# Performance work log

Hardware: AMD Instinct MI355X
Metric: run time of the kernel (lower is better)

The kernel has to match this reference:

```python
import jax, jax.numpy as jnp
import numpy as np

N, S, E, H = 2, 2048, 1024, 16
D = E // H  # head_dim = 64


def setup_inputs() -> dict:
    key = jax.random.key(0)
    k1, k2, k3 = jax.random.split(key, 3)
    x = jax.random.normal(k1, (N, S, E), dtype=jnp.float32)
    # Xavier-uniform-scaled weights (torch Linear layout: [out_features, in_features])
    lim_qkv = (6.0 / (E + 3 * E)) ** 0.5
    qkv_w = jax.random.uniform(k2, (3 * E, E), dtype=jnp.float32, minval=-lim_qkv, maxval=lim_qkv)
    lim_o = (6.0 / (E + E)) ** 0.5
    o_w = jax.random.uniform(k3, (E, E), dtype=jnp.float32, minval=-lim_o, maxval=lim_o)
    # causal look-ahead mask: positions where mask == 0 are excluded
    attn_mask = jnp.tril(jnp.ones((S, S), dtype=jnp.int32))
    return {"x": x, "attn_mask": attn_mask, "qkv_w": qkv_w, "o_w": o_w}


def reference(x, attn_mask, qkv_w, o_w):
    n, s, e = x.shape
    qkv = x @ qkv_w.T                              # (N, S, 3E)
    q, k, v = jnp.split(qkv, 3, axis=-1)
    # (N, S, E) -> (N, H, S, D)
    def to_heads(t):
        return t.reshape(n, s, H, D).transpose(0, 2, 1, 3)
    q, k, v = to_heads(q), to_heads(k), to_heads(v)
    scale = 1.0 / jnp.sqrt(jnp.asarray(D, dtype=x.dtype))
    logits = jnp.einsum('bhqd,bhkd->bhqk', q, k) * scale   # (N, H, S, S)
    mask = attn_mask.reshape(1, 1, s, s)                    # expand_mask: 2D -> (1,1,S,S)
    logits = jnp.where(mask == 0, -jnp.inf, logits)
    attn_weights = jax.nn.softmax(logits, axis=-1)
    values = jnp.einsum('bhqk,bhkd->bhqd', attn_weights, v)  # (N, H, S, D)
    values = values.transpose(0, 2, 1, 3).reshape(n, s, e)
    o = values @ o_w.T
    return o
```

## Files before the change

### kernel.cpp

```cpp
#include <hip/hip_runtime.h>
#include <math.h>

typedef unsigned short u16;
typedef unsigned int uint;
typedef __attribute__((ext_vector_type(8))) short bf16x8;
typedef __attribute__((ext_vector_type(8))) _Float16 half8;
typedef __attribute__((ext_vector_type(4))) float floatx4;

__device__ __forceinline__ u16 f2bf(float f) {
  union { float f; uint u; } c; c.f = f;
  return (u16)((c.u + 0x7FFFu + ((c.u >> 16) & 1u)) >> 16);
}
__device__ __forceinline__ float bf2f(u16 h) {
  union { uint u; float f; } c; c.u = ((uint)h) << 16;
  return c.f;
}
__device__ __forceinline__ u16 h2u(_Float16 h) {
  union { _Float16 h; u16 u; } c; c.h = h;
  return c.u;
}

#if __has_builtin(__builtin_amdgcn_exp2f)
#define EX2 __builtin_amdgcn_exp2f
#else
#define EX2 exp2f
#endif

__device__ __forceinline__ void gl_lds16(const u16* g, u16* l) {
  __builtin_amdgcn_global_load_lds(
      (const __attribute__((address_space(1))) uint*)g,
      (__attribute__((address_space(3))) uint*)l, 16, 0, 0);
}

__device__ __forceinline__ void store_c(u16* p, float v) { *p = f2bf(v); }
__device__ __forceinline__ void store_c(float* p, float v) { *p = v; }

#define ROR16(x, n)                                                        \
  __builtin_bit_cast(float, __builtin_amdgcn_update_dpp(                   \
      __builtin_bit_cast(int, (x)), __builtin_bit_cast(int, (x)),          \
      0x120 + (n), 0xF, 0xF, false))
__device__ __forceinline__ float rsum16(float x) {
  x += ROR16(x, 8); x += ROR16(x, 4); x += ROR16(x, 2); x += ROR16(x, 1);
  return x;
}

__global__ __launch_bounds__(256) void cvt_all(const float* __restrict__ x,
                                               const float* __restrict__ qw,
                                               const float* __restrict__ ow,
                                               u16* __restrict__ xb,
                                               u16* __restrict__ wb,
                                               u16* __restrict__ ob) {
  int bx = blockIdx.x;
  const float* src; u16* dst; int off;
  if (bx < 2048) { src = x; dst = xb; off = bx; }
  else if (bx < 3584) { src = qw; dst = wb; off = bx - 2048; }
  else { src = ow; dst = ob; off = bx - 3584; }
  int i = (off * 256 + threadIdx.x) * 8;
  float4 a = *(const float4*)(src + i);
  float4 b = *(const float4*)(src + i + 4);
  bf16x8 r;
  r[0] = (short)f2bf(a.x); r[1] = (short)f2bf(a.y);
  r[2] = (short)f2bf(a.z); r[3] = (short)f2bf(a.w);
  r[4] = (short)f2bf(b.x); r[5] = (short)f2bf(b.y);
  r[6] = (short)f2bf(b.z); r[7] = (short)f2bf(b.w);
  *(bf16x8*)(dst + i) = r;
}

__global__ __launch_bounds__(256) void vtrans(const u16* __restrict__ qkv,
                                              u16* __restrict__ vt) {
  constexpr int S = 2048, E = 1024, TE = 3072;
  __shared__ u16 tile[64 * 72];
  const int t = threadIdx.x;
  const int kv0 = blockIdx.x * 64;
  const int bh = blockIdx.y, b = bh >> 4, h = bh & 15;
  const u16* src = qkv + (size_t)b * S * TE + 2 * E + h * 64;
#pragma unroll
  for (int i = 0; i < 2; ++i) {
    int c = t + i * 256;
    int kv = c >> 3, d0 = (c & 7) * 8;
    *(bf16x8*)&tile[kv * 72 + d0] = *(const bf16x8*)&src[(size_t)(kv0 + kv) * TE + d0];
  }
  __syncthreads();
  u16* dst = vt + (size_t)bh * 64 * S + kv0;
#pragma unroll
  for (int i = 0; i < 2; ++i) {
    int c = t + i * 256;
    int d = c >> 3, k0 = (c & 7) * 8;
    bf16x8 r;
#pragma unroll
    for (int j = 0; j < 8; ++j)
      r[j] = (short)h2u((_Float16)bf2f(tile[(k0 + j) * 72 + d]));
    *(bf16x8*)&dst[(size_t)d * S + k0] = r;
  }
}

template <typename TC>
__global__ __launch_bounds__(256) void gemm_bt(const u16* __restrict__ A,
                                               const u16* __restrict__ B,
                                               TC* __restrict__ C,
                                               int K, int N) {
  __shared__ __align__(16) u16 lds_a[128 * 64];
  __shared__ __align__(16) u16 lds_b[128 * 64];
  const int t = threadIdx.x;
  const int w = t >> 6, lane = t & 63, quad = lane >> 4, lr = lane & 15;
  const int wr = w >> 1, wc = w & 1;
  const int m0 = blockIdx.y * 128, n0 = blockIdx.x * 128;

  const int srow = lane >> 3;
  const int scol = ((lane & 7) ^ srow) * 8;
  const u16* Ab = A + (size_t)(m0 + w * 32 + srow) * K + scol;
  const u16* Bb = B + (size_t)(n0 + w * 32 + srow) * K + scol;
  u16* la = lds_a + (w * 32) * 64;
  u16* lb = lds_b + (w * 32) * 64;

  floatx4 acc[4][4];
#pragma unroll
  for (int i = 0; i < 4; ++i)
#pragma unroll
    for (int j = 0; j < 4; ++j) acc[i][j] = {0.f, 0.f, 0.f, 0.f};

  for (int k0 = 0; k0 < K; k0 += 64) {
#pragma unroll
    for (int j = 0; j < 4; ++j) {
      gl_lds16(Ab + (size_t)(j * 8) * K + k0, la + j * 8 * 64);
      gl_lds16(Bb + (size_t)(j * 8) * K + k0, lb + j * 8 * 64);
    }
    __syncthreads();
#pragma unroll
    for (int kk = 0; kk < 2; ++kk) {
      bf16x8 af[4], bfr[4];
#pragma unroll
      for (int mi = 0; mi < 4; ++mi)
        af[mi] = *(const bf16x8*)&lds_a[(wr * 64 + mi * 16 + lr) * 64 +
                                        (((kk * 4 + quad) ^ (lr & 7)) * 8)];
#pragma unroll
      for (int ni = 0; ni < 4; ++ni)
        bfr[ni] = *(const bf16x8*)&lds_b[(wc * 64 + ni * 16 + lr) * 64 +
                                         (((kk * 4 + quad) ^ (lr & 7)) * 8)];
#pragma unroll
      for (int mi = 0; mi < 4; ++mi)
#pragma unroll
        for (int ni = 0; ni < 4; ++ni)
          acc[mi][ni] = __builtin_amdgcn_mfma_f32_16x16x32_bf16(
              af[mi], bfr[ni], acc[mi][ni], 0, 0, 0);
    }
    __syncthreads();
  }
#pragma unroll
  for (int mi = 0; mi < 4; ++mi)
#pragma unroll
    for (int r = 0; r < 4; ++r) {
      int m = m0 + wr * 64 + mi * 16 + quad * 4 + r;
#pragma unroll
      for (int ni = 0; ni < 4; ++ni) {
        int n = n0 + wc * 64 + ni * 16 + lr;
        store_c(&C[(size_t)m * N + n], acc[mi][ni][r]);
      }
    }
}

template <typename TC>
__global__ __launch_bounds__(256) void gemm_bt64(const u16* __restrict__ A,
                                                 const u16* __restrict__ B,
                                                 TC* __restrict__ C,
                                                 int K, int N) {
  __shared__ __align__(16) u16 lds_a[64 * 64];
  __shared__ __align__(16) u16 lds_b[128 * 64];
  const int t = threadIdx.x;
  const int w = t >> 6, lane = t & 63, quad = lane >> 4, lr = lane & 15;
  const int m0 = blockIdx.y * 64, n0 = blockIdx.x * 128;

  const int srow = lane >> 3;
  const int scol = ((lane & 7) ^ srow) * 8;
  const u16* Ab = A + (size_t)(m0 + srow) * K + scol;
  const u16* Bb = B + (size_t)(n0 + srow) * K + scol;

  floatx4 acc[4][2];
#pragma unroll
  for (int i = 0; i < 4; ++i)
#pragma unroll
    for (int j = 0; j < 2; ++j) acc[i][j] = {0.f, 0.f, 0.f, 0.f};

  for (int k0 = 0; k0 < K; k0 += 64) {
#pragma unroll
    for (int i = 0; i < 2; ++i)
      gl_lds16(Ab + (size_t)((w * 2 + i) * 8) * K + k0, &lds_a[(w * 2 + i) * 8 * 64]);
#pragma unroll
    for (int i = 0; i < 4; ++i)
      gl_lds16(Bb + (size_t)((w * 4 + i) * 8) * K + k0, &lds_b[(w * 4 + i) * 8 * 64]);
    __syncthreads();
#pragma unroll
    for (int kk = 0; kk < 2; ++kk) {
      bf16x8 af[4], bfr[2];
#pragma unroll
      for (int mi = 0; mi < 4; ++mi)
        af[mi] = *(const bf16x8*)&lds_a[(mi * 16 + lr) * 64 +
                                        (((kk * 4 + quad) ^ (lr & 7)) * 8)];
#pragma unroll
      for (int ni = 0; ni < 2; ++ni)
        bfr[ni] = *(const bf16x8*)&lds_b[(w * 32 + ni * 16 + lr) * 64 +
                                         (((kk * 4 + quad) ^ (lr & 7)) * 8)];
#pragma unroll
      for (int mi = 0; mi < 4; ++mi)
#pragma unroll
        for (int ni = 0; ni < 2; ++ni)
          acc[mi][ni] = __builtin_amdgcn_mfma_f32_16x16x32_bf16(
              af[mi], bfr[ni], acc[mi][ni], 0, 0, 0);
    }
    __syncthreads();
  }
#pragma unroll
  for (int mi = 0; mi < 4; ++mi)
#pragma unroll
    for (int r = 0; r < 4; ++r) {
      int m = m0 + mi * 16 + quad * 4 + r;
#pragma unroll
      for (int ni = 0; ni < 2; ++ni) {
        int n = n0 + w * 32 + ni * 16 + lr;
        store_c(&C[(size_t)m * N + n], acc[mi][ni][r]);
      }
    }
}

__global__ __launch_bounds__(256, 2) void attn_fwd(const u16* __restrict__ qkv,
                                                   const u16* __restrict__ vt,
                                                   u16* __restrict__ out,
                                                   float* __restrict__ opart,
                                                   float* __restrict__ lpart) {
  constexpr int S = 2048, E = 1024, TE = 3072;
  constexpr float NEG = -1e30f;
  __shared__ __align__(16) u16 lds_k[2][128 * 64];
  __shared__ __align__(16) u16 lds_vt[2][64 * 128];
  __shared__ __align__(16) u16 lds_p[4][16 * 128];
  const int t = threadIdx.x;
  const int w = t >> 6, lane = t & 63, quad = lane >> 4, lr = lane & 15;
  const int bx = (int)blockIdx.x;
  const int h = bx & 15, pr = (bx >> 4) & 7, hB = (bx >> 7) & 1, b = bx >> 8;
  const int qtH = 15 - pr;
  const int bh = b * 16 + h;
  const int pid = bh * 8 + pr;
  const size_t base = (size_t)b * S * TE;
  const u16* kbase = qkv + base + E + h * 64;
  const u16* vtb = vt + (size_t)bh * 64 * S;

  const int s8 = lane >> 3;
  const int kcol = ((lane & 7) ^ s8) * 8;
  const int vrow = lane >> 4;
  u16* const pb = &lds_p[w][0];

  const int n0 = hB ? (8 - pr) : 8;
  const int niter = hB ? 9 : 8;

  const float QS = 0.125f * 1.44269504f;
  bf16x8 qf[2][2];
  float lst[2][4];
  floatx4 oacc[2][4];

  auto load_q = [&](int qt) {
#pragma unroll
    for (int rg = 0; rg < 2; ++rg)
#pragma unroll
      for (int kk = 0; kk < 2; ++kk) {
        bf16x8 q = *(const bf16x8*)&qkv[base +
            (size_t)(qt * 128 + w * 32 + rg * 16 + lr) * TE + h * 64 + kk * 32 + quad * 8];
#pragma unroll
        for (int jj = 0; jj < 8; ++jj) q[jj] = (short)f2bf(bf2f((u16)q[jj]) * QS);
        qf[rg][kk] = q;
      }
  };
  auto reset_acc = [&]() {
#pragma unroll
    for (int rg = 0; rg < 2; ++rg) {
#pragma unroll
      for (int r = 0; r < 4; ++r) lst[rg][r] = 0.f;
#pragma unroll
      for (int di = 0; di < 4; ++di) oacc[rg][di] = {0.f, 0.f, 0.f, 0.f};
    }
  };
  auto emit_partial = [&](int slot) {
    float* op = opart + ((size_t)slot * 256 + pid) * (128 * 64);
    float* lp = lpart + ((size_t)slot * 256 + pid) * 128;
#pragma unroll
    for (int rg = 0; rg < 2; ++rg)
#pragma unroll
      for (int r = 0; r < 4; ++r) {
        int row = w * 32 + rg * 16 + quad * 4 + r;
        float lt = rsum16(lst[rg][r]);
        if (lr == 0) lp[row] = lt;
#pragma unroll
        for (int di = 0; di < 4; ++di)
          op[row * 64 + di * 16 + lr] = oacc[rg][di][r];
      }
  };
  auto kv_of = [&](int it) -> int {
    if (!hB) return it;
    return (it < n0) ? (8 + it) : (it - n0);
  };
  auto stage = [&](int kvt, int bi) {
    int nb = kvt * 128;
#pragma unroll
    for (int i = 0; i < 4; ++i) {
      int p0 = w * 8 + i * 32;
      int kv = nb + ((p0 & 15) + s8) * 8 + (p0 >> 4);
      gl_lds16(kbase + (size_t)kv * TE + kcol, &lds_k[bi][p0 * 64]);
    }
#pragma unroll
    for (int i = 0; i < 4; ++i) {
      int d0 = w * 4 + i * 16;
      int d = d0 + vrow;
      int cbg = ((lane & 15) ^ (d & 15)) * 8;
      gl_lds16(vtb + (size_t)d * S + nb + cbg, &lds_vt[bi][d0 * 128]);
    }
  };

  load_q(qtH);
  stage(kv_of(0), 0);
  reset_acc();

  for (int it = 0; it < niter; ++it) {
    const int cur = it & 1;
    const int kt = kv_of(it);
    const int qcur = (hB && it >= n0) ? pr : qtH;

    if (it + 1 < niter) {
      stage(kv_of(it + 1), cur ^ 1);
      asm volatile("s_waitcnt vmcnt(8)\n\ts_barrier" ::: "memory");
    } else {
      asm volatile("s_waitcnt vmcnt(0)\n\ts_barrier" ::: "memory");
    }
    __builtin_amdgcn_sched_barrier(0);

    floatx4 st[2][8];
#pragma unroll
    for (int rg = 0; rg < 2; ++rg)
#pragma unroll
      for (int ni = 0; ni < 8; ++ni) st[rg][ni] = {-4.f, -4.f, -4.f, -4.f};
    __builtin_amdgcn_s_setprio(1);
#pragma unroll
    for (int kk = 0; kk < 2; ++kk) {
      bf16x8 kb[8];
#pragma unroll
      for (int ni = 0; ni < 8; ++ni)
        kb[ni] = *(const bf16x8*)&lds_k[cur][(ni * 16 + lr) * 64 +
                                            (((kk * 4 + quad) ^ (lr & 7)) * 8)];
#pragma unroll
      for (int rg = 0; rg < 2; ++rg)
#pragma unroll
        for (int ni = 0; ni < 8; ++ni)
          st[rg][ni] = __builtin_amdgcn_mfma_f32_16x16x32_bf16(
              qf[rg][kk], kb[ni], st[rg][ni], 0, 0, 0);
    }
    __builtin_amdgcn_s_setprio(0);

    half8 vb[4][4];
#pragma unroll
    for (int kk = 0; kk < 4; ++kk)
#pragma unroll
      for (int di = 0; di < 4; ++di)
        vb[kk][di] = *(const half8*)&lds_vt[cur][(di * 16 + lr) * 128 +
                                                 (((kk * 4 + quad) ^ lr) << 3)];

    asm volatile("s_waitcnt lgkmcnt(0)\n\ts_barrier" ::: "memory");
    __builtin_amdgcn_sched_barrier(0);

    const bool diag = (kt == qcur);
#pragma unroll
    for (int rg = 0; rg < 2; ++rg) {
#pragma unroll
      for (int r = 0; r < 4; ++r) {
        const int rw = quad * 4 + r;
        const int rloc = w * 32 + rg * 16 + rw;
        if (diag) {
#pragma unroll
          for (int ni = 0; ni < 8; ++ni)
            if (lr * 8 + ni > rloc) st[rg][ni][r] = NEG;
        }
        float pv[8];
#pragma unroll
        for (int ni = 0; ni < 8; ++ni) pv[ni] = EX2(st[rg][ni][r]);
        lst[rg][r] += ((pv[0] + pv[1]) + (pv[2] + pv[3])) +
                      ((pv[4] + pv[5]) + (pv[6] + pv[7]));
        half8 p8;
#pragma unroll
        for (int ni = 0; ni < 8; ++ni) p8[ni] = (_Float16)pv[ni];
        *(half8*)&pb[rw * 128 + (((lr + rw) & 15) << 3)] = p8;
      }
      __builtin_amdgcn_s_setprio(1);
#pragma unroll
      for (int kk = 0; kk < 4; ++kk) {
        half8 pf = *(const half8*)&pb[lr * 128 +
                                      ((((kk * 4 + quad) + lr) & 15) << 3)];
#pragma unroll
        for (int di = 0; di < 4; ++di)
          oacc[rg][di] = __builtin_amdgcn_mfma_f32_16x16x32_f16(
              pf, vb[kk][di], oacc[rg][di], 0, 0, 0);
      }
      __builtin_amdgcn_s_setprio(0);
    }

    if (hB && it == n0 - 1) {
      emit_partial(1);
      reset_acc();
      load_q(pr);
    }
  }

  if (!hB) {
    emit_partial(0);
  } else {
#pragma unroll
    for (int rg = 0; rg < 2; ++rg)
#pragma unroll
      for (int r = 0; r < 4; ++r) {
        int sg = pr * 128 + w * 32 + rg * 16 + quad * 4 + r;
        float inv_l = 1.f / rsum16(lst[rg][r]);
#pragma unroll
        for (int di = 0; di < 4; ++di)
          out[((size_t)(b * S + sg)) * E + h * 64 + di * 16 + lr] =
              f2bf(oacc[rg][di][r] * inv_l);
      }
  }
}

__global__ __launch_bounds__(256) void attn_combine(const float* __restrict__ opart,
                                                    const float* __restrict__ lpart,
                                                    u16* __restrict__ out) {
  constexpr int S = 2048, E = 1024;
  const int p = (int)blockIdx.x;
  const int pr = p & 7, bh = p >> 3, h = bh & 15, b = bh >> 4;
  const int q0 = (15 - pr) * 128;
  const int t = threadIdx.x;
  const int row = t >> 1, c0 = (t & 1) * 32;
  const float* o0 = opart + (size_t)p * (128 * 64) + row * 64 + c0;
  const float* o1 = o0 + (size_t)256 * 128 * 64;
  float l = lpart[p * 128 + row] + lpart[256 * 128 + p * 128 + row];
  float inv = 1.f / l;
  u16* dst = out + ((size_t)(b * S + q0 + row)) * E + h * 64 + c0;
#pragma unroll
  for (int i = 0; i < 4; ++i) {
    float4 a0 = ((const float4*)o0)[2 * i], a1 = ((const float4*)o0)[2 * i + 1];
    float4 b0 = ((const float4*)o1)[2 * i], b1 = ((const float4*)o1)[2 * i + 1];
    bf16x8 r;
    r[0] = (short)f2bf((a0.x + b0.x) * inv);
    r[1] = (short)f2bf((a0.y + b0.y) * inv);
    r[2] = (short)f2bf((a0.z + b0.z) * inv);
    r[3] = (short)f2bf((a0.w + b0.w) * inv);
    r[4] = (short)f2bf((a1.x + b1.x) * inv);
    r[5] = (short)f2bf((a1.y + b1.y) * inv);
    r[6] = (short)f2bf((a1.z + b1.z) * inv);
    r[7] = (short)f2bf((a1.w + b1.w) * inv);
    ((bf16x8*)dst)[i] = r;
  }
}

extern "C" void kernel_launch(void* const* d_in, const int* in_sizes, int n_in,
                              void* d_out, int out_size, void* d_ws, size_t ws_size,
                              hipStream_t stream) {
  constexpr int NB = 2, S = 2048, E = 1024;
  constexpr int M = NB * S;
  const float* x = (const float*)d_in[0];
  const float* qkv_w = (const float*)d_in[2];
  const float* o_w = (const float*)d_in[3];
  float* out = (float*)d_out;

  u16* qkv = (u16*)d_ws;
  u16* vt = qkv + (size_t)M * 3 * E;
  u16* xb = vt + (size_t)32 * 64 * S;
  u16* attn_o = xb;
  u16* wb = xb + (size_t)M * E;
  u16* ob = wb + (size_t)3 * E * E;
  float* opart = (float*)(ob + (size_t)E * E);
  float* lpart = opart + (size_t)2 * 256 * 128 * 64;

  cvt_all<<<4096, 256, 0, stream>>>(x, qkv_w, o_w, xb, wb, ob);
  gemm_bt<u16><<<dim3(3 * E / 128, M / 128), 256, 0, stream>>>(xb, wb, qkv, E, 3 * E);
  vtrans<<<dim3(S / 64, NB * 16), 256, 0, stream>>>(qkv, vt);
  attn_fwd<<<512, 256, 0, stream>>>(qkv, vt, attn_o, opart, lpart);
  attn_combine<<<256, 256, 0, stream>>>(opart, lpart, attn_o);
  gemm_bt64<float><<<dim3(E / 128, M / 64), 256, 0, stream>>>(attn_o, ob, out, E, E);
}
```

Baseline: 184.3 us.

## Compute transposed QK^T to keep P in registers, drop LDS round-trip

The QK^T MFMA operands are swapped so each lane holds scores for one query row across several keys. K rows are staged in a permuted order so those register values line up with the A-operand layout of the PV MFMA. The P matrix is then packed to fp16 in registers with cvt_pkrtz instead of being written to and read back from LDS. Row sums are kept per lane and reduced with two shuffles only at the end. The prefetch of the next KV tile now issues after the V fragment reads, with a full vmcnt(0) wait at the top of each iteration, which can expose more load latency.

```diff
diff --git a/kernel.cpp b/kernel.cpp
--- a/kernel.cpp
+++ b/kernel.cpp
@@ -5,6 +5,7 @@
 typedef unsigned int uint;
 typedef __attribute__((ext_vector_type(8))) short bf16x8;
 typedef __attribute__((ext_vector_type(8))) _Float16 half8;
+typedef __attribute__((ext_vector_type(2))) _Float16 half2t;
 typedef __attribute__((ext_vector_type(4))) float floatx4;
 
 __device__ __forceinline__ u16 f2bf(float f) {
@@ -231,7 +232,6 @@
   constexpr float NEG = -1e30f;
   __shared__ __align__(16) u16 lds_k[2][128 * 64];
   __shared__ __align__(16) u16 lds_vt[2][64 * 128];
-  __shared__ __align__(16) u16 lds_p[4][16 * 128];
   const int t = threadIdx.x;
   const int w = t >> 6, lane = t & 63, quad = lane >> 4, lr = lane & 15;
   const int bx = (int)blockIdx.x;
@@ -246,14 +246,13 @@
   const int s8 = lane >> 3;
   const int kcol = ((lane & 7) ^ s8) * 8;
   const int vrow = lane >> 4;
-  u16* const pb = &lds_p[w][0];
 
   const int n0 = hB ? (8 - pr) : 8;
   const int niter = hB ? 9 : 8;
 
   const float QS = 0.125f * 1.44269504f;
   bf16x8 qf[2][2];
-  float lst[2][4];
+  float lst2[2];
   floatx4 oacc[2][4];
 
   auto load_q = [&](int qt) {
@@ -269,24 +268,33 @@
       }
   };
   auto reset_acc = [&]() {
+    lst2[0] = 0.f; lst2[1] = 0.f;
+#pragma unroll
+    for (int rg = 0; rg < 2; ++rg)
+#pragma unroll
+      for (int di = 0; di < 4; ++di) oacc[rg][di] = {0.f, 0.f, 0.f, 0.f};
+  };
+  auto reduce_l = [&](float* lred) {
 #pragma unroll
     for (int rg = 0; rg < 2; ++rg) {
-#pragma unroll
-      for (int r = 0; r < 4; ++r) lst[rg][r] = 0.f;
-#pragma unroll
-      for (int di = 0; di < 4; ++di) oacc[rg][di] = {0.f, 0.f, 0.f, 0.f};
+      float x = lst2[rg];
+      x += __shfl_xor(x, 16);
+      x += __shfl_xor(x, 32);
+      lred[rg] = x;
     }
   };
   auto emit_partial = [&](int slot) {
+    float lred[2];
+    reduce_l(lred);
     float* op = opart + ((size_t)slot * 256 + pid) * (128 * 64);
     float* lp = lpart + ((size_t)slot * 256 + pid) * 128;
+    if (quad == 0) lp[w * 32 + lr] = lred[0];
+    if (quad == 1) lp[w * 32 + 16 + lr] = lred[1];
 #pragma unroll
     for (int rg = 0; rg < 2; ++rg)
 #pragma unroll
       for (int r = 0; r < 4; ++r) {
         int row = w * 32 + rg * 16 + quad * 4 + r;
-        float lt = rsum16(lst[rg][r]);
-        if (lr == 0) lp[row] = lt;
 #pragma unroll
         for (int di = 0; di < 4; ++di)
           op[row * 64 + di * 16 + lr] = oacc[rg][di][r];
@@ -301,8 +309,9 @@
 #pragma unroll
     for (int i = 0; i < 4; ++i) {
       int p0 = w * 8 + i * 32;
-      int kv = nb + ((p0 & 15) + s8) * 8 + (p0 >> 4);
-      gl_lds16(kbase + (size_t)kv * TE + kcol, &lds_k[bi][p0 * 64]);
+      int p = p0 + s8;
+      int kv = ((p >> 5) & 3) * 32 + ((p >> 2) & 3) * 8 + ((p >> 4) & 1) * 4 + (p & 3);
+      gl_lds16(kbase + (size_t)(nb + kv) * TE + kcol, &lds_k[bi][p0 * 64]);
     }
 #pragma unroll
     for (int i = 0; i < 4; ++i) {
@@ -322,12 +331,7 @@
     const int kt = kv_of(it);
     const int qcur = (hB && it >= n0) ? pr : qtH;
 
-    if (it + 1 < niter) {
-      stage(kv_of(it + 1), cur ^ 1);
-      asm volatile("s_waitcnt vmcnt(8)\n\ts_barrier" ::: "memory");
-    } else {
-      asm volatile("s_waitcnt vmcnt(0)\n\ts_barrier" ::: "memory");
-    }
+    asm volatile("s_waitcnt vmcnt(0)\n\ts_barrier" ::: "memory");
     __builtin_amdgcn_sched_barrier(0);
 
     floatx4 st[2][8];
@@ -348,7 +352,7 @@
 #pragma unroll
         for (int ni = 0; ni < 8; ++ni)
           st[rg][ni] = __builtin_amdgcn_mfma_f32_16x16x32_bf16(
-              qf[rg][kk], kb[ni], st[rg][ni], 0, 0, 0);
+              kb[ni], qf[rg][kk], st[rg][ni], 0, 0, 0);
     }
     __builtin_amdgcn_s_setprio(0);
 
@@ -360,40 +364,46 @@
         vb[kk][di] = *(const half8*)&lds_vt[cur][(di * 16 + lr) * 128 +
                                                  (((kk * 4 + quad) ^ lr) << 3)];
 
-    asm volatile("s_waitcnt lgkmcnt(0)\n\ts_barrier" ::: "memory");
-    __builtin_amdgcn_sched_barrier(0);
+    if (it + 1 < niter) stage(kv_of(it + 1), cur ^ 1);
 
     const bool diag = (kt == qcur);
 #pragma unroll
     for (int rg = 0; rg < 2; ++rg) {
-#pragma unroll
-      for (int r = 0; r < 4; ++r) {
-        const int rw = quad * 4 + r;
-        const int rloc = w * 32 + rg * 16 + rw;
-        if (diag) {
-#pragma unroll
-          for (int ni = 0; ni < 8; ++ni)
-            if (lr * 8 + ni > rloc) st[rg][ni][r] = NEG;
+      const int rloc = w * 32 + rg * 16 + lr;
+      float ex[8][4];
+#pragma unroll
+      for (int ni = 0; ni < 8; ++ni)
+#pragma unroll
+        for (int rr = 0; rr < 4; ++rr) {
+          float s = st[rg][ni][rr];
+          if (diag) {
+            int kvl = ((ni >> 1) << 5) + (quad << 3) + ((ni & 1) << 2) + rr;
+            if (kvl > rloc) s = NEG;
+          }
+          ex[ni][rr] = EX2(s);
         }
-        float pv[8];
-#pragma unroll
-        for (int ni = 0; ni < 8; ++ni) pv[ni] = EX2(st[rg][ni][r]);
-        lst[rg][r] += ((pv[0] + pv[1]) + (pv[2] + pv[3])) +
-                      ((pv[4] + pv[5]) + (pv[6] + pv[7]));
-        half8 p8;
-#pragma unroll
-        for (int ni = 0; ni < 8; ++ni) p8[ni] = (_Float16)pv[ni];
-        *(half8*)&pb[rw * 128 + (((lr + rw) & 15) << 3)] = p8;
-      }
+      float tsum[8];
+#pragma unroll
+      for (int ni = 0; ni < 8; ++ni)
+        tsum[ni] = (ex[ni][0] + ex[ni][1]) + (ex[ni][2] + ex[ni][3]);
+      lst2[rg] += ((tsum[0] + tsum[1]) + (tsum[2] + tsum[3])) +
+                  ((tsum[4] + tsum[5]) + (tsum[6] + tsum[7]));
       __builtin_amdgcn_s_setprio(1);
 #pragma unroll
-      for (int kk = 0; kk < 4; ++kk) {
-        half8 pf = *(const half8*)&pb[lr * 128 +
-                                      ((((kk * 4 + quad) + lr) & 15) << 3)];
+      for (int c = 0; c < 4; ++c) {
+        union { half2t h2[4]; half8 h8; } pu;
+        pu.h2[0] = __builtin_bit_cast(half2t,
+            __builtin_amdgcn_cvt_pkrtz(ex[2 * c][0], ex[2 * c][1]));
+        pu.h2[1] = __builtin_bit_cast(half2t,
+            __builtin_amdgcn_cvt_pkrtz(ex[2 * c][2], ex[2 * c][3]));
+        pu.h2[2] = __builtin_bit_cast(half2t,
+            __builtin_amdgcn_cvt_pkrtz(ex[2 * c + 1][0], ex[2 * c + 1][1]));
+        pu.h2[3] = __builtin_bit_cast(half2t,
+            __builtin_amdgcn_cvt_pkrtz(ex[2 * c + 1][2], ex[2 * c + 1][3]));
 #pragma unroll
         for (int di = 0; di < 4; ++di)
           oacc[rg][di] = __builtin_amdgcn_mfma_f32_16x16x32_f16(
-              pf, vb[kk][di], oacc[rg][di], 0, 0, 0);
+              pu.h8, vb[c][di], oacc[rg][di], 0, 0, 0);
       }
       __builtin_amdgcn_s_setprio(0);
     }
@@ -408,12 +418,15 @@
   if (!hB) {
     emit_partial(0);
   } else {
+    float lred[2];
+    reduce_l(lred);
 #pragma unroll
     for (int rg = 0; rg < 2; ++rg)
 #pragma unroll
       for (int r = 0; r < 4; ++r) {
         int sg = pr * 128 + w * 32 + rg * 16 + quad * 4 + r;
-        float inv_l = 1.f / rsum16(lst[rg][r]);
+        float lrow = __shfl(lred[rg], quad * 4 + r);
+        float inv_l = 1.f / lrow;
 #pragma unroll
         for (int di = 0; di < 4; ++di)
           out[((size_t)(b * S + sg)) * E + h * 64 + di * 16 + lr] =
```

New measurement: 198.6 us. 1.08x slower.
